# Kernel optimization log

Hardware: AMD Instinct MI355X
Metric: run time of the kernel (lower is better)

Reference implementation:

```python
import jax, jax.numpy as jnp
import numpy as np

N_NODES = 100000
N_EDGES = 1600000
NUM_GRAPHS = 128
FLAVOURS = 17
C = 32


def setup_inputs() -> dict:
    key = jax.random.key(0)
    ks = jax.random.split(key, 12)
    return {
        "x_idx": jax.random.randint(ks[0], (N_NODES,), 0, FLAVOURS),
        "edge_index": jax.random.randint(ks[1], (2, N_EDGES), 0, N_NODES),
        "batch": jnp.sort(jax.random.randint(ks[2], (N_NODES,), 0, NUM_GRAPHS)),
        "embed_w": jax.random.normal(ks[3], (FLAVOURS, C), jnp.float32),
        "conv_w": jax.random.normal(ks[4], (5, C, C), jnp.float32) * 0.2,
        "conv_b": jax.random.normal(ks[5], (5, C), jnp.float32) * 0.1,
        "d0_w": jax.random.normal(ks[6], (C, C), jnp.float32) * 0.2,
        "d0_b": jax.random.normal(ks[7], (C,), jnp.float32) * 0.1,
        "dense_w": jax.random.normal(ks[8], (3, C, C), jnp.float32) * 0.2,
        "dense_b": jax.random.normal(ks[9], (3, C), jnp.float32) * 0.1,
        "fin_w": jax.random.normal(ks[10], (2, C), jnp.float32) * 0.2,
        "fin_b": jax.random.normal(ks[11], (2,), jnp.float32) * 0.1,
    }


def reference(x_idx, edge_index, batch, embed_w, conv_w, conv_b,
              d0_w, d0_b, dense_w, dense_b, fin_w, fin_b):
    n = x_idx.shape[0]
    loops = jnp.arange(n)
    src = jnp.concatenate([edge_index[0], loops])  # message sources (x_j)
    dst = jnp.concatenate([edge_index[1], loops])  # aggregation targets
    # GCN symmetric normalization with self-loops: deg^-1/2 A_hat deg^-1/2
    deg = jax.ops.segment_sum(jnp.ones_like(dst, dtype=jnp.float32), dst,
                              num_segments=n)
    dinv = jax.lax.rsqrt(deg)  # deg >= 1 thanks to self-loops
    norm = dinv[src] * dinv[dst]  # [E+N]

    h = embed_w[x_idx]  # [N, C]
    for l in range(5):
        z = h @ conv_w[l].T                      # linear transform
        msgs = norm[:, None] * z[src]            # gather + scale
        agg = jax.ops.segment_sum(msgs, dst, num_segments=n) + conv_b[l]
        h = jax.nn.relu(agg)                     # dropout is identity in eval

    pooled = jax.ops.segment_max(h, batch, num_segments=NUM_GRAPHS)  # [G, C]
    pooled = jnp.where(jnp.isfinite(pooled), pooled, 0.0)  # guard empty graphs

    y = jax.nn.relu(pooled @ d0_w.T + d0_b)
    for l in range(3):
        y = jax.nn.relu(y @ dense_w[l].T + dense_b[l])
    logits = y @ fin_w.T + fin_b  # [G, 2]
    return jax.nn.log_softmax(logits, axis=1)
```

## Files before the change

kernel.cpp:

```cpp
#include <hip/hip_runtime.h>
#include <hip/hip_bf16.h>
#include <hip/hip_fp16.h>


#define CDIM 32
#define BSHIFT 7
#define BSPAN 128
#define MAXBUK 800
#define CHUNK 12800
#define BCAP 2560
#define CSRCAP 3072

__global__ void __launch_bounds__(256) bin_count(
    const int* __restrict__ edst, int* __restrict__ counts, int E, int nbuk) {
    __shared__ int hist[MAXBUK];
    int t = threadIdx.x;
    int base = blockIdx.x * CHUNK;
    int n = min(CHUNK, E - base);
    for (int i = t; i < nbuk; i += 256) hist[i] = 0;
    __syncthreads();
    for (int i = t; i < n; i += 256)
        atomicAdd(&hist[edst[base + i] >> BSHIFT], 1);
    __syncthreads();
    for (int b = t; b < nbuk; b += 256)
        counts[blockIdx.x * MAXBUK + b] = hist[b];
}

__global__ void __launch_bounds__(256) colscan(
    const int* __restrict__ counts, int* __restrict__ runpre,
    int* __restrict__ btot, int nchunks) {
    __shared__ int s[256];
    int b = blockIdx.x, t = threadIdx.x;
    int v = (t < nchunks) ? counts[t * MAXBUK + b] : 0;
    s[t] = v;
    __syncthreads();
    for (int d = 1; d < 256; d <<= 1) {
        int x = (t >= d) ? s[t - d] : 0;
        __syncthreads();
        s[t] += x;
        __syncthreads();
    }
    if (t < nchunks) runpre[t * MAXBUK + b] = s[t] - v;
    if (t == 255) btot[b] = s[255];
}

__global__ void __launch_bounds__(256) bin_scatter(
    const int* __restrict__ esrc, const int* __restrict__ edst,
    const int* __restrict__ runpre, unsigned* __restrict__ pairs,
    int E, int nbuk) {
    __shared__ int lcur[MAXBUK];
    int t = threadIdx.x;
    int base = blockIdx.x * CHUNK;
    int n = min(CHUNK, E - base);
    for (int b = t; b < nbuk; b += 256)
        lcur[b] = runpre[blockIdx.x * MAXBUK + b];
    __syncthreads();
    for (int i = t; i < n; i += 256) {
        int d = edst[base + i];
        int s = esrc[base + i];
        int b = d >> BSHIFT;
        int pos = atomicAdd(&lcur[b], 1);
        pairs[(size_t)b * BCAP + pos] =
            ((unsigned)(d & (BSPAN - 1)) << 20) | (unsigned)s;
    }
}

__global__ void __launch_bounds__(256) build_csr(
    const unsigned* __restrict__ pairs, const int* __restrict__ btot,
    int* __restrict__ cnt, float* __restrict__ dinvx,
    int* __restrict__ offsets4, int* __restrict__ csr, int N) {
    __shared__ int h[BSPAN];
    __shared__ int p[BSPAN];
    __shared__ int lcur[BSPAN];
    __shared__ int obase[BSPAN];
    int b = blockIdx.x, t = threadIdx.x;
    if (t < BSPAN) h[t] = 0;
    __syncthreads();
    size_t p0 = (size_t)b * BCAP;
    size_t p1 = p0 + btot[b];
    for (size_t i = p0 + t; i < p1; i += 256)
        atomicAdd(&h[pairs[i] >> 20], 1);
    __syncthreads();
    int own = 0;
    if (t < BSPAN) {
        int v = (b << BSHIFT) + t;
        int c = (v < N) ? h[t] : 0;
        if (v < N) {
            cnt[v] = c;
            dinvx[v] = rsqrtf((float)c + 1.0f);
        }
        own = (c + 3) & ~3;
        p[t] = own;
    }
    __syncthreads();
    for (int d = 1; d < BSPAN; d <<= 1) {
        int x = 0;
        if (t < BSPAN && t >= d) x = p[t - d];
        __syncthreads();
        if (t < BSPAN) p[t] += x;
        __syncthreads();
    }
    if (t < BSPAN) {
        int o = b * CSRCAP + p[t] - own;
        int v = (b << BSHIFT) + t;
        if (v < N) offsets4[v] = o;
        lcur[t] = o;
        obase[t] = o;
    }
    if (b == 0 && t == 255) dinvx[N] = 0.f;
    __syncthreads();
    for (size_t i = p0 + t; i < p1; i += 256) {
        unsigned pk = pairs[i];
        int pos = atomicAdd(&lcur[pk >> 20], 1);
        csr[pos] = (int)(pk & 0xFFFFFu);
    }
    __syncthreads();
    if (t < BSPAN) {
        int v = (b << BSHIFT) + t;
        if (v < N) {
            int e = lcur[t];
            int e1 = obase[t] + ((e - obase[t] + 3) & ~3);
            for (; e < e1; ++e) csr[e] = N;
        }
    }
}

__global__ void embed_half(const int* __restrict__ x_idx, const float* __restrict__ ew,
                           const float* __restrict__ dinvx,
                           __half* __restrict__ hA, __half* __restrict__ hB, int N) {
    int tid = blockIdx.x * 256 + threadIdx.x;
    int i = tid >> 5;
    int c = tid & 31;
    if (i > N) return;
    if (i == N) {
        hA[tid] = __float2half(0.f);
        hB[tid] = __float2half(0.f);
        return;
    }
    hA[tid] = __float2half(dinvx[i] * ew[x_idx[i] * CDIM + c]);
}

__global__ void __launch_bounds__(256) gcn_layer(
    const __half* __restrict__ ht, const float* __restrict__ dinvx,
    const int* __restrict__ offsets4, const int* __restrict__ cnt,
    const int* __restrict__ csr, const float* __restrict__ W,
    const float* __restrict__ bias, __half* __restrict__ out,
    int N, int scale_next) {
    int c = threadIdx.x & 31;
    int grp = threadIdx.x >> 5;

    float w[CDIM];
    {
        const float4* Wrow = reinterpret_cast<const float4*>(W + c * CDIM);
        #pragma unroll
        for (int q = 0; q < CDIM / 4; ++q) {
            float4 t = Wrow[q];
            w[4 * q + 0] = t.x;
            w[4 * q + 1] = t.y;
            w[4 * q + 2] = t.z;
            w[4 * q + 3] = t.w;
        }
    }
    float bc = bias[c];

    for (int v0 = blockIdx.x * 8; v0 < N; v0 += gridDim.x * 8) {
        int v = v0 + grp;
        if (v >= N) continue;
        float dv = dinvx[v];
        float acc = __half2float(ht[v * CDIM + c]);
        int e = offsets4[v];
        int e1 = e + ((cnt[v] + 3) & ~3);
        for (; e < e1; e += 4) {
            int4 s4 = *reinterpret_cast<const int4*>(&csr[e]);
            float a0 = __half2float(ht[s4.x * CDIM + c]);
            float a1 = __half2float(ht[s4.y * CDIM + c]);
            float a2 = __half2float(ht[s4.z * CDIM + c]);
            float a3 = __half2float(ht[s4.w * CDIM + c]);
            acc += (a0 + a1) + (a2 + a3);
        }
        float aggv = dv * acc;
        float o = bc;
        #pragma unroll
        for (int k = 0; k < CDIM; ++k)
            o = fmaf(__shfl(aggv, k, 32), w[k], o);
        o = fmaxf(o, 0.f);
        if (scale_next) o *= dv;
        out[v * CDIM + c] = __float2half(o);
    }
}

#define PCHUNK 128
__global__ void pool_kernel(const __half* __restrict__ h, const int* __restrict__ batch,
                            unsigned* __restrict__ pooled, int N) {
    __shared__ int sb[8 * PCHUNK];
    int t = threadIdx.x;
    int chunk0 = blockIdx.x * 8;
    int sbase = chunk0 * PCHUNK;
    for (int i = t; i < 8 * PCHUNK; i += 256)
        sb[i] = (sbase + i < N) ? batch[sbase + i] : -1;
    __syncthreads();
    int c = t & 31, cs = t >> 5;
    int i0 = (chunk0 + cs) * PCHUNK;
    if (i0 >= N) return;
    int curg = sb[cs * PCHUNK];
    float m = -1.0f;
    for (int k = 0; k < PCHUNK; ++k) {
        int i = i0 + k;
        if (i >= N) break;
        int g = sb[cs * PCHUNK + k];
        float v = __half2float(h[i * CDIM + c]);
        if (g != curg) {
            if (m >= 0.f) atomicMax(&pooled[curg * CDIM + c], __float_as_uint(m));
            curg = g;
            m = v;
        } else {
            m = fmaxf(m, v);
        }
    }
    if (m >= 0.f && curg >= 0) atomicMax(&pooled[curg * CDIM + c], __float_as_uint(m));
}

__global__ void __launch_bounds__(256) head_kernel(
    const float* __restrict__ pooled,
    const float* __restrict__ d0_w, const float* __restrict__ d0_b,
    const float* __restrict__ dense_w, const float* __restrict__ dense_b,
    const float* __restrict__ fin_w, const float* __restrict__ fin_b,
    float* __restrict__ out, int G) {
    int c = threadIdx.x & 31;
    int grp = threadIdx.x >> 5;
    int g = blockIdx.x * 8 + grp;
    if (g >= G) return;

    float x = pooled[g * CDIM + c];

    const float* Ws[4] = {d0_w, dense_w, dense_w + CDIM * CDIM,
                          dense_w + 2 * CDIM * CDIM};
    const float* bs[4] = {d0_b, dense_b, dense_b + CDIM, dense_b + 2 * CDIM};
    for (int l = 0; l < 4; ++l) {
        float w[CDIM];
        const float4* Wrow = reinterpret_cast<const float4*>(Ws[l] + c * CDIM);
        #pragma unroll
        for (int q = 0; q < CDIM / 4; ++q) {
            float4 t = Wrow[q];
            w[4 * q + 0] = t.x;
            w[4 * q + 1] = t.y;
            w[4 * q + 2] = t.z;
            w[4 * q + 3] = t.w;
        }
        float acc = bs[l][c];
        #pragma unroll
        for (int k = 0; k < CDIM; ++k)
            acc = fmaf(__shfl(x, k, 32), w[k], acc);
        x = fmaxf(acc, 0.f);
    }
    float p0 = x * fin_w[c];
    float p1 = x * fin_w[CDIM + c];
    #pragma unroll
    for (int d = 16; d > 0; d >>= 1) {
        p0 += __shfl_xor(p0, d, 32);
        p1 += __shfl_xor(p1, d, 32);
    }
    float l0 = p0 + fin_b[0], l1 = p1 + fin_b[1];
    float mm = fmaxf(l0, l1);
    float lse = mm + logf(expf(l0 - mm) + expf(l1 - mm));
    if (c == 0) {
        out[g * 2 + 0] = l0 - lse;
        out[g * 2 + 1] = l1 - lse;
    }
}

extern "C" void kernel_launch(void* const* d_in, const int* in_sizes, int n_in,
                              void* d_out, int out_size, void* d_ws, size_t ws_size,
                              hipStream_t stream) {
    const int* x_idx = (const int*)d_in[0];
    const int* eidx = (const int*)d_in[1];
    const int* batch = (const int*)d_in[2];
    const float* embed_w = (const float*)d_in[3];
    const float* conv_w = (const float*)d_in[4];
    const float* conv_b = (const float*)d_in[5];
    const float* d0_w = (const float*)d_in[6];
    const float* d0_b = (const float*)d_in[7];
    const float* dense_w = (const float*)d_in[8];
    const float* dense_b = (const float*)d_in[9];
    const float* fin_w = (const float*)d_in[10];
    const float* fin_b = (const float*)d_in[11];

    int N = in_sizes[0];
    int E = in_sizes[1] / 2;
    int G = out_size / 2;
    const int* esrc = eidx;
    const int* edst = eidx + E;
    int nbuk = (N + BSPAN - 1) >> BSHIFT;
    int CB = (E + CHUNK - 1) / CHUNK;

    char* ws = (char*)d_ws;
    size_t off = 0;
    auto take = [&](size_t bytes) -> char* {
        char* p = ws + off;
        off = (off + bytes + 255) & ~(size_t)255;
        return p;
    };
    int* cnt = (int*)take((size_t)N * 4);
    float* dinvx = (float*)take((size_t)(N + 1) * 4);
    int* offsets4 = (int*)take((size_t)N * 4);
    int* btot = (int*)take(MAXBUK * 4);
    int* counts = (int*)take((size_t)CB * MAXBUK * 4);
    int* runpre = (int*)take((size_t)CB * MAXBUK * 4);
    unsigned* pairs = (unsigned*)take((size_t)MAXBUK * BCAP * 4);
    int* csr = (int*)take((size_t)MAXBUK * CSRCAP * 4);
    __half* hA = (__half*)take((size_t)(N + 1) * CDIM * 2);
    __half* hB = (__half*)take((size_t)(N + 1) * CDIM * 2);
    unsigned* pooled = (unsigned*)take((size_t)G * CDIM * 4);
    (void)ws_size;
    (void)n_in;

    hipMemsetAsync(pooled, 0, (size_t)G * CDIM * 4, stream);

    bin_count<<<CB, 256, 0, stream>>>(edst, counts, E, nbuk);
    colscan<<<nbuk, 256, 0, stream>>>(counts, runpre, btot, CB);
    bin_scatter<<<CB, 256, 0, stream>>>(esrc, edst, runpre, pairs, E, nbuk);
    build_csr<<<nbuk, 256, 0, stream>>>(pairs, btot, cnt, dinvx, offsets4, csr, N);

    embed_half<<<((N + 1) * CDIM + 255) / 256, 256, 0, stream>>>(
        x_idx, embed_w, dinvx, hA, hB, N);

    int LB = 2048;
    gcn_layer<<<LB, 256, 0, stream>>>(hA, dinvx, offsets4, cnt, csr,
                                      conv_w + 0 * CDIM * CDIM, conv_b + 0 * CDIM, hB, N, 1);
    gcn_layer<<<LB, 256, 0, stream>>>(hB, dinvx, offsets4, cnt, csr,
                                      conv_w + 1 * CDIM * CDIM, conv_b + 1 * CDIM, hA, N, 1);
    gcn_layer<<<LB, 256, 0, stream>>>(hA, dinvx, offsets4, cnt, csr,
                                      conv_w + 2 * CDIM * CDIM, conv_b + 2 * CDIM, hB, N, 1);
    gcn_layer<<<LB, 256, 0, stream>>>(hB, dinvx, offsets4, cnt, csr,
                                      conv_w + 3 * CDIM * CDIM, conv_b + 3 * CDIM, hA, N, 1);
    gcn_layer<<<LB, 256, 0, stream>>>(hA, dinvx, offsets4, cnt, csr,
                                      conv_w + 4 * CDIM * CDIM, conv_b + 4 * CDIM, hB, N, 0);

    int nchunks = (N + PCHUNK - 1) / PCHUNK;
    pool_kernel<<<(nchunks + 7) / 8, 256, 0, stream>>>(hB, batch, pooled, N);
    head_kernel<<<(G + 7) / 8, 256, 0, stream>>>((const float*)pooled, d0_w, d0_b,
                                                 dense_w, dense_b, fin_w, fin_b,
                                                 (float*)d_out, G);
}
```

Baseline: 321.0 us.

## Fuse embed into CSR build, pool with head, and drop memset launch

Cuts launch count in three places. The embedding lookup is folded into the CSR build kernel, which reuses the per-node dinv values it already holds in shared memory. The pooled buffer is zeroed inside bin_count instead of by a separate memset. Pooling and the dense head are merged using a last-block-done atomic counter, so the single finishing block runs the MLP head. This removes three launches and their inter-kernel gaps, but the head now runs serially in one block, and correctness depends on the threadfence and atomic counter ordering.

```diff
diff --git a/kernel.cpp b/kernel.cpp
--- a/kernel.cpp
+++ b/kernel.cpp
@@ -10,11 +10,18 @@
 #define CHUNK 12800
 #define BCAP 2560
 #define CSRCAP 3072
+#define PCHUNK 128
 
 __global__ void __launch_bounds__(256) bin_count(
-    const int* __restrict__ edst, int* __restrict__ counts, int E, int nbuk) {
+    const int* __restrict__ edst, int* __restrict__ counts,
+    unsigned* __restrict__ pooled, int* __restrict__ done,
+    int E, int nbuk, int G) {
     __shared__ int hist[MAXBUK];
     int t = threadIdx.x;
+    if (blockIdx.x == 0) {
+        for (int i = t; i < G * CDIM; i += 256) pooled[i] = 0u;
+        if (t == 0) *done = 0;
+    }
     int base = blockIdx.x * CHUNK;
     int n = min(CHUNK, E - base);
     for (int i = t; i < nbuk; i += 256) hist[i] = 0;
@@ -65,15 +72,19 @@
     }
 }
 
-__global__ void __launch_bounds__(256) build_csr(
+__global__ void __launch_bounds__(256) build_csr_embed(
     const unsigned* __restrict__ pairs, const int* __restrict__ btot,
+    const int* __restrict__ x_idx, const float* __restrict__ ew,
     int* __restrict__ cnt, float* __restrict__ dinvx,
-    int* __restrict__ offsets4, int* __restrict__ csr, int N) {
+    int* __restrict__ offsets4, int* __restrict__ csr,
+    __half* __restrict__ hA, __half* __restrict__ hB, int N) {
     __shared__ int h[BSPAN];
     __shared__ int p[BSPAN];
     __shared__ int lcur[BSPAN];
     __shared__ int obase[BSPAN];
+    __shared__ int xi[BSPAN];
     int b = blockIdx.x, t = threadIdx.x;
+    int v0 = b << BSHIFT;
     if (t < BSPAN) h[t] = 0;
     __syncthreads();
     size_t p0 = (size_t)b * BCAP;
@@ -83,12 +94,15 @@
     __syncthreads();
     int own = 0;
     if (t < BSPAN) {
-        int v = (b << BSHIFT) + t;
+        int v = v0 + t;
         int c = (v < N) ? h[t] : 0;
+        float dv = rsqrtf((float)c + 1.0f);
         if (v < N) {
             cnt[v] = c;
-            dinvx[v] = rsqrtf((float)c + 1.0f);
-        }
+            dinvx[v] = dv;
+            xi[t] = x_idx[v];
+        }
+        h[t] = __float_as_int(dv);
         own = (c + 3) & ~3;
         p[t] = own;
     }
@@ -102,12 +116,11 @@
     }
     if (t < BSPAN) {
         int o = b * CSRCAP + p[t] - own;
-        int v = (b << BSHIFT) + t;
+        int v = v0 + t;
         if (v < N) offsets4[v] = o;
         lcur[t] = o;
         obase[t] = o;
     }
-    if (b == 0 && t == 255) dinvx[N] = 0.f;
     __syncthreads();
     for (size_t i = p0 + t; i < p1; i += 256) {
         unsigned pk = pairs[i];
@@ -116,28 +129,27 @@
     }
     __syncthreads();
     if (t < BSPAN) {
-        int v = (b << BSHIFT) + t;
+        int v = v0 + t;
         if (v < N) {
             int e = lcur[t];
             int e1 = obase[t] + ((e - obase[t] + 3) & ~3);
             for (; e < e1; ++e) csr[e] = N;
         }
     }
-}
-
-__global__ void embed_half(const int* __restrict__ x_idx, const float* __restrict__ ew,
-                           const float* __restrict__ dinvx,
-                           __half* __restrict__ hA, __half* __restrict__ hB, int N) {
-    int tid = blockIdx.x * 256 + threadIdx.x;
-    int i = tid >> 5;
-    int c = tid & 31;
-    if (i > N) return;
-    if (i == N) {
-        hA[tid] = __float2half(0.f);
-        hB[tid] = __float2half(0.f);
-        return;
-    }
-    hA[tid] = __float2half(dinvx[i] * ew[x_idx[i] * CDIM + c]);
+    for (int idx = t; idx < BSPAN * CDIM; idx += 256) {
+        int dl = idx >> 5;
+        int v = v0 + dl;
+        if (v < N) {
+            float dv = __int_as_float(h[dl]);
+            hA[v * CDIM + (idx & 31)] =
+                __float2half(dv * ew[xi[dl] * CDIM + (idx & 31)]);
+        }
+    }
+    if (b == 0 && t < CDIM) {
+        dinvx[N] = 0.f;
+        hA[N * CDIM + t] = __float2half(0.f);
+        hB[N * CDIM + t] = __float2half(0.f);
+    }
 }
 
 __global__ void __launch_bounds__(256) gcn_layer(
@@ -189,10 +201,15 @@
     }
 }
 
-#define PCHUNK 128
-__global__ void pool_kernel(const __half* __restrict__ h, const int* __restrict__ batch,
-                            unsigned* __restrict__ pooled, int N) {
+__global__ void __launch_bounds__(256) pool_head(
+    const __half* __restrict__ h, const int* __restrict__ batch,
+    unsigned* __restrict__ pooled, int* __restrict__ done,
+    const float* __restrict__ d0_w, const float* __restrict__ d0_b,
+    const float* __restrict__ dense_w, const float* __restrict__ dense_b,
+    const float* __restrict__ fin_w, const float* __restrict__ fin_b,
+    float* __restrict__ out, int N, int G) {
     __shared__ int sb[8 * PCHUNK];
+    __shared__ int is_last;
     int t = threadIdx.x;
     int chunk0 = blockIdx.x * 8;
     int sbase = chunk0 * PCHUNK;
@@ -201,71 +218,70 @@
     __syncthreads();
     int c = t & 31, cs = t >> 5;
     int i0 = (chunk0 + cs) * PCHUNK;
-    if (i0 >= N) return;
-    int curg = sb[cs * PCHUNK];
-    float m = -1.0f;
-    for (int k = 0; k < PCHUNK; ++k) {
-        int i = i0 + k;
-        if (i >= N) break;
-        int g = sb[cs * PCHUNK + k];
-        float v = __half2float(h[i * CDIM + c]);
-        if (g != curg) {
-            if (m >= 0.f) atomicMax(&pooled[curg * CDIM + c], __float_as_uint(m));
-            curg = g;
-            m = v;
-        } else {
-            m = fmaxf(m, v);
-        }
-    }
-    if (m >= 0.f && curg >= 0) atomicMax(&pooled[curg * CDIM + c], __float_as_uint(m));
-}
-
-__global__ void __launch_bounds__(256) head_kernel(
-    const float* __restrict__ pooled,
-    const float* __restrict__ d0_w, const float* __restrict__ d0_b,
-    const float* __restrict__ dense_w, const float* __restrict__ dense_b,
-    const float* __restrict__ fin_w, const float* __restrict__ fin_b,
-    float* __restrict__ out, int G) {
-    int c = threadIdx.x & 31;
-    int grp = threadIdx.x >> 5;
-    int g = blockIdx.x * 8 + grp;
-    if (g >= G) return;
-
-    float x = pooled[g * CDIM + c];
-
-    const float* Ws[4] = {d0_w, dense_w, dense_w + CDIM * CDIM,
-                          dense_w + 2 * CDIM * CDIM};
-    const float* bs[4] = {d0_b, dense_b, dense_b + CDIM, dense_b + 2 * CDIM};
-    for (int l = 0; l < 4; ++l) {
-        float w[CDIM];
-        const float4* Wrow = reinterpret_cast<const float4*>(Ws[l] + c * CDIM);
+    if (i0 < N) {
+        int curg = sb[cs * PCHUNK];
+        float m = -1.0f;
+        for (int k = 0; k < PCHUNK; ++k) {
+            int i = i0 + k;
+            if (i >= N) break;
+            int g = sb[cs * PCHUNK + k];
+            float v = __half2float(h[i * CDIM + c]);
+            if (g != curg) {
+                if (m >= 0.f) atomicMax(&pooled[curg * CDIM + c], __float_as_uint(m));
+                curg = g;
+                m = v;
+            } else {
+                m = fmaxf(m, v);
+            }
+        }
+        if (m >= 0.f && curg >= 0) atomicMax(&pooled[curg * CDIM + c], __float_as_uint(m));
+    }
+    __syncthreads();
+    if (t == 0) {
+        __threadfence();
+        int old = atomicAdd(done, 1);
+        is_last = (old == (int)gridDim.x - 1) ? 1 : 0;
+    }
+    __syncthreads();
+    if (!is_last) return;
+
+    int grp = t >> 5;
+    for (int g = grp; g < G; g += 8) {
+        float x = __uint_as_float(atomicMax(&pooled[g * CDIM + c], 0u));
+        const float* Ws[4] = {d0_w, dense_w, dense_w + CDIM * CDIM,
+                              dense_w + 2 * CDIM * CDIM};
+        const float* bs[4] = {d0_b, dense_b, dense_b + CDIM, dense_b + 2 * CDIM};
+        for (int l = 0; l < 4; ++l) {
+            float w[CDIM];
+            const float4* Wrow = reinterpret_cast<const float4*>(Ws[l] + c * CDIM);
+            #pragma unroll
+            for (int q = 0; q < CDIM / 4; ++q) {
+                float4 tv = Wrow[q];
+                w[4 * q + 0] = tv.x;
+                w[4 * q + 1] = tv.y;
+                w[4 * q + 2] = tv.z;
+                w[4 * q + 3] = tv.w;
+            }
+            float acc = bs[l][c];
+            #pragma unroll
+            for (int k = 0; k < CDIM; ++k)
+                acc = fmaf(__shfl(x, k, 32), w[k], acc);
+            x = fmaxf(acc, 0.f);
+        }
+        float p0 = x * fin_w[c];
+        float p1 = x * fin_w[CDIM + c];
         #pragma unroll
-        for (int q = 0; q < CDIM / 4; ++q) {
-            float4 t = Wrow[q];
-            w[4 * q + 0] = t.x;
-            w[4 * q + 1] = t.y;
-            w[4 * q + 2] = t.z;
-            w[4 * q + 3] = t.w;
-        }
-        float acc = bs[l][c];
-        #pragma unroll
-        for (int k = 0; k < CDIM; ++k)
-            acc = fmaf(__shfl(x, k, 32), w[k], acc);
-        x = fmaxf(acc, 0.f);
-    }
-    float p0 = x * fin_w[c];
-    float p1 = x * fin_w[CDIM + c];
-    #pragma unroll
-    for (int d = 16; d > 0; d >>= 1) {
-        p0 += __shfl_xor(p0, d, 32);
-        p1 += __shfl_xor(p1, d, 32);
-    }
-    float l0 = p0 + fin_b[0], l1 = p1 + fin_b[1];
-    float mm = fmaxf(l0, l1);
-    float lse = mm + logf(expf(l0 - mm) + expf(l1 - mm));
-    if (c == 0) {
-        out[g * 2 + 0] = l0 - lse;
-        out[g * 2 + 1] = l1 - lse;
+        for (int d = 16; d > 0; d >>= 1) {
+            p0 += __shfl_xor(p0, d, 32);
+            p1 += __shfl_xor(p1, d, 32);
+        }
+        float l0 = p0 + fin_b[0], l1 = p1 + fin_b[1];
+        float mm = fmaxf(l0, l1);
+        float lse = mm + logf(expf(l0 - mm) + expf(l1 - mm));
+        if (c == 0) {
+            out[g * 2 + 0] = l0 - lse;
+            out[g * 2 + 1] = l1 - lse;
+        }
     }
 }
 
@@ -304,6 +320,7 @@
     float* dinvx = (float*)take((size_t)(N + 1) * 4);
     int* offsets4 = (int*)take((size_t)N * 4);
     int* btot = (int*)take(MAXBUK * 4);
+    int* done = (int*)take(256);
     int* counts = (int*)take((size_t)CB * MAXBUK * 4);
     int* runpre = (int*)take((size_t)CB * MAXBUK * 4);
     unsigned* pairs = (unsigned*)take((size_t)MAXBUK * BCAP * 4);
@@ -314,15 +331,11 @@
     (void)ws_size;
     (void)n_in;
 
-    hipMemsetAsync(pooled, 0, (size_t)G * CDIM * 4, stream);
-
-    bin_count<<<CB, 256, 0, stream>>>(edst, counts, E, nbuk);
+    bin_count<<<CB, 256, 0, stream>>>(edst, counts, pooled, done, E, nbuk, G);
     colscan<<<nbuk, 256, 0, stream>>>(counts, runpre, btot, CB);
     bin_scatter<<<CB, 256, 0, stream>>>(esrc, edst, runpre, pairs, E, nbuk);
-    build_csr<<<nbuk, 256, 0, stream>>>(pairs, btot, cnt, dinvx, offsets4, csr, N);
-
-    embed_half<<<((N + 1) * CDIM + 255) / 256, 256, 0, stream>>>(
-        x_idx, embed_w, dinvx, hA, hB, N);
+    build_csr_embed<<<nbuk, 256, 0, stream>>>(pairs, btot, x_idx, embed_w,
+                                              cnt, dinvx, offsets4, csr, hA, hB, N);
 
     int LB = 2048;
     gcn_layer<<<LB, 256, 0, stream>>>(hA, dinvx, offsets4, cnt, csr,
@@ -337,8 +350,7 @@
                                       conv_w + 4 * CDIM * CDIM, conv_b + 4 * CDIM, hB, N, 0);
 
     int nchunks = (N + PCHUNK - 1) / PCHUNK;
-    pool_kernel<<<(nchunks + 7) / 8, 256, 0, stream>>>(hB, batch, pooled, N);
-    head_kernel<<<(G + 7) / 8, 256, 0, stream>>>((const float*)pooled, d0_w, d0_b,
-                                                 dense_w, dense_b, fin_w, fin_b,
-                                                 (float*)d_out, G);
-}
+    pool_head<<<(nchunks + 7) / 8, 256, 0, stream>>>(
+        hB, batch, pooled, done, d0_w, d0_b, dense_w, dense_b, fin_w, fin_b,
+        (float*)d_out, N, G);
+}
```

New measurement: 376.1 us. +17.2%, slower.
